# Optimization experiments

Hardware: AMD Instinct MI355X
Metric: run time of the kernel (lower is better)

## Reference

```python
import jax, jax.numpy as jnp
import numpy as np

B, T, C, H, L, E, K, V = 4, 1024, 1024, 16, 2, 8, 2, 32000
HD = C // H
CAP = B * T * K // E  # expert capacity with capacity_factor=1.0 -> 2048


def setup_inputs() -> dict:
    key = jax.random.key(0)
    ks = iter(jax.random.split(key, 16))
    def rn(shape, s=0.02):
        return jax.random.normal(next(ks), shape, jnp.float32) * s
    return {
        'input_ids': jax.random.randint(next(ks), (B, T), 0, V),
        'noise': jax.random.normal(next(ks), (L, B, T, E), jnp.float32),
        'tok_emb': rn((V, C)),
        'pos_emb': rn((T, C)),
        'ln1_w': jnp.ones((L, C)), 'ln1_b': jnp.zeros((L, C)),
        'qkv_w': rn((L, 3 * C, C)), 'out_w': rn((L, C, C)),
        'ln2_w': jnp.ones((L, C)), 'ln2_b': jnp.zeros((L, C)),
        'rt_w': rn((L, E, C)), 'rt_b': jnp.zeros((L, E)),
        'nz_w': rn((L, E, C)), 'nz_b': jnp.zeros((L, E)),
        'e_w1': rn((L, E, 4 * C, C)), 'e_b1': jnp.zeros((L, E, 4 * C)),
        'e_w2': rn((L, E, C, 4 * C)), 'e_b2': jnp.zeros((L, E, C)),
        'lnf_w': jnp.ones((C,)), 'lnf_b': jnp.zeros((C,)),
        'head_w': rn((1, C)), 'head_b': jnp.zeros((1,)),
    }


def _ln(x, w, b):
    m = jnp.mean(x, -1, keepdims=True)
    v = jnp.mean(jnp.square(x - m), -1, keepdims=True)
    return (x - m) * jax.lax.rsqrt(v + 1e-5) * w + b


def _attn(x, qkv_w, out_w):
    # non-causal flash-attention equivalent (softmax_scale = 1/sqrt(head_size))
    qkv = (x @ qkv_w.T).reshape(B, T, 3, H, HD)
    q, k, v = qkv[:, :, 0], qkv[:, :, 1], qkv[:, :, 2]
    s = jnp.einsum('bthd,bshd->bhts', q, k) / np.float32(np.sqrt(HD))
    p = jax.nn.softmax(s, axis=-1)
    o = jnp.einsum('bhts,bshd->bthd', p, v).reshape(B, T, C)
    return o @ out_w.T


def _moe(x, rt_w, rt_b, nz_w, nz_b, w1, b1, w2, b2, noise):
    logits = x @ rt_w.T + rt_b                      # [B,T,E]
    noise_logits = x @ nz_w.T + nz_b
    noisy = logits + noise * jax.nn.softplus(noise_logits)
    topv, topi = jax.lax.top_k(noisy, K)            # [B,T,K]
    gates = jax.nn.softmax(topv, axis=-1)           # softmax over sparse (-inf filled) logits == softmax over top-k
    oh = jax.nn.one_hot(topi, E, dtype=x.dtype)     # [B,T,K,E]
    router = jnp.einsum('btk,btke->bte', gates, oh)
    N = B * T
    flat_x = x.reshape(N, C)
    flat_r = router.reshape(N, E)
    flat_i = topi.reshape(N, K)
    updates = jnp.zeros_like(flat_x)
    for i in range(E):  # per-expert gather -> FFN -> scatter, capacity-limited in token order
        mask = jnp.any(flat_i == i, axis=-1)        # [N]
        pos = jnp.cumsum(mask) - 1
        keep = mask & (pos < CAP)
        sel = jnp.argsort(jnp.logical_not(keep))[:CAP]  # stable: kept tokens first, original order
        valid = keep[sel].astype(x.dtype)
        xi = flat_x[sel]                             # [CAP,C]
        h = jax.nn.relu(xi @ w1[i].T + b1[i])
        out = h @ w2[i].T + b2[i]
        gate = flat_r[sel, i] * valid
        updates = updates.at[sel].add(out * gate[:, None])
    return updates.reshape(B, T, C)


def reference(input_ids, noise, tok_emb, pos_emb, ln1_w, ln1_b, qkv_w, out_w,
              ln2_w, ln2_b, rt_w, rt_b, nz_w, nz_b, e_w1, e_b1, e_w2, e_b2,
              lnf_w, lnf_b, head_w, head_b):
    x = tok_emb[input_ids] + pos_emb[None, :T]
    for l in range(L):
        x = x + _attn(_ln(x, ln1_w[l], ln1_b[l]), qkv_w[l], out_w[l])
        x = x + _moe(_ln(x, ln2_w[l], ln2_b[l]), rt_w[l], rt_b[l], nz_w[l], nz_b[l],
                     e_w1[l], e_b1[l], e_w2[l], e_b2[l], noise[l])
    x = _ln(x, lnf_w, lnf_b)
    return jnp.mean(x, axis=1) @ head_w.T + head_b  # [B,1]
```

## Files before the change

kernel.cpp:

```cpp
#include <hip/hip_runtime.h>
#include <hip/hip_bf16.h>
#include <math.h>

namespace {

constexpr int B = 4, T = 1024, C = 1024, Hh = 16, L = 2, E = 8, HD = 64;
constexpr int NTOK = B * T;
constexpr int CAP = 1024;
constexpr int C3 = 3 * C, C4 = 4 * C;

typedef __attribute__((ext_vector_type(8))) short bf16x8;
typedef __attribute__((ext_vector_type(8))) short short8;
typedef __attribute__((ext_vector_type(4))) float f32x4;

static __device__ __forceinline__ short f2b(float f) {
  __hip_bfloat16 h = __float2bfloat16(f);
  return *reinterpret_cast<short*>(&h);
}
static __device__ __forceinline__ float b2f(unsigned short u) {
  union { unsigned int i; float f; } v; v.i = (unsigned int)u << 16; return v.f;
}

#define SWZ(row, kb) (((row) << 7) + ((kb) ^ (((row) & 7) << 4)))

static __device__ __forceinline__ void gload16(const void* g, void* l) {
  __builtin_amdgcn_global_load_lds((const __attribute__((address_space(1))) void*)g,
                                   (__attribute__((address_space(3))) void*)l, 16, 0, 0);
}

__global__ __launch_bounds__(256) void cvt4_kernel(
    const float* __restrict__ s0, const float* __restrict__ s1,
    const float* __restrict__ s2, const float* __restrict__ s3,
    unsigned short* __restrict__ d0, unsigned short* __restrict__ d1,
    unsigned short* __restrict__ d2, unsigned short* __restrict__ d3) {
  constexpr size_t N0 = (size_t)L * C3 * C, N1 = (size_t)L * C * C;
  constexpr size_t N2 = (size_t)L * E * C4 * C;
  size_t i = ((size_t)blockIdx.x * 256 + threadIdx.x) * 16;
  const float* s; unsigned short* d; size_t off;
  if (i < N0)                { s = s0; d = d0; off = i; }
  else if (i < N0 + N1)      { s = s1; d = d1; off = i - N0; }
  else if (i < N0 + N1 + N2) { s = s2; d = d2; off = i - N0 - N1; }
  else                       { s = s3; d = d3; off = i - N0 - N1 - N2; }
  f32x4 v0 = __builtin_nontemporal_load((const f32x4*)(s + off));
  f32x4 v1 = __builtin_nontemporal_load((const f32x4*)(s + off + 4));
  f32x4 v2 = __builtin_nontemporal_load((const f32x4*)(s + off + 8));
  f32x4 v3 = __builtin_nontemporal_load((const f32x4*)(s + off + 12));
  short8 r0, r1;
  r0[0] = f2b(v0[0]); r0[1] = f2b(v0[1]); r0[2] = f2b(v0[2]); r0[3] = f2b(v0[3]);
  r0[4] = f2b(v1[0]); r0[5] = f2b(v1[1]); r0[6] = f2b(v1[2]); r0[7] = f2b(v1[3]);
  r1[0] = f2b(v2[0]); r1[1] = f2b(v2[1]); r1[2] = f2b(v2[2]); r1[3] = f2b(v2[3]);
  r1[4] = f2b(v3[0]); r1[5] = f2b(v3[1]); r1[6] = f2b(v3[2]); r1[7] = f2b(v3[3]);
  __builtin_nontemporal_store(r0, (short8*)(d + off));
  __builtin_nontemporal_store(r1, (short8*)(d + off + 8));
}

__global__ __launch_bounds__(256) void embed_ln_kernel(const int* __restrict__ ids,
    const float* __restrict__ tok, const float* __restrict__ pos,
    float* __restrict__ x, unsigned short* __restrict__ outb,
    const float* __restrict__ w, const float* __restrict__ b) {
  __shared__ float red[8];
  int row = blockIdx.x, tid = threadIdx.x;
  int t = row & (T - 1);
  int id = ids[row];
  float4 a = ((const float4*)(tok + (size_t)id * C))[tid];
  float4 p = ((const float4*)(pos + (size_t)t * C))[tid];
  float4 v{a.x + p.x, a.y + p.y, a.z + p.z, a.w + p.w};
  ((float4*)(x + (size_t)row * C))[tid] = v;
  float s = v.x + v.y + v.z + v.w;
  #pragma unroll
  for (int off = 32; off > 0; off >>= 1) s += __shfl_down(s, off);
  if ((tid & 63) == 0) red[tid >> 6] = s;
  __syncthreads();
  float mean = (red[0] + red[1] + red[2] + red[3]) * (1.f / C);
  __syncthreads();
  float dx = v.x - mean, dy = v.y - mean, dz = v.z - mean, dw = v.w - mean;
  float sq = dx * dx + dy * dy + dz * dz + dw * dw;
  #pragma unroll
  for (int off = 32; off > 0; off >>= 1) sq += __shfl_down(sq, off);
  if ((tid & 63) == 0) red[tid >> 6] = sq;
  __syncthreads();
  float var = (red[0] + red[1] + red[2] + red[3]) * (1.f / C);
  float rs = rsqrtf(var + 1e-5f);
  float4 wc = ((const float4*)w)[tid];
  float4 bc = ((const float4*)b)[tid];
  short4 ob{f2b(dx * rs * wc.x + bc.x), f2b(dy * rs * wc.y + bc.y),
            f2b(dz * rs * wc.z + bc.z), f2b(dw * rs * wc.w + bc.w)};
  *(short4*)(outb + (size_t)row * C + tid * 4) = ob;
}

__global__ __launch_bounds__(256) void ln_kernel(const float* __restrict__ in,
    const unsigned short* __restrict__ eo, const int* __restrict__ slot0,
    const int* __restrict__ slot1, float* __restrict__ xupd,
    float* __restrict__ out, unsigned short* __restrict__ outb,
    const float* __restrict__ w, const float* __restrict__ b) {
  constexpr size_t SLICE = (size_t)E * CAP * C;
  __shared__ float red[8];
  int row = blockIdx.x, tid = threadIdx.x;
  float4 v = ((const float4*)(in + (size_t)row * C))[tid];
  if (eo) {
    int s0 = slot0[row], s1 = slot1[row];
    auto addslot = [&](int s) {
      if (s < 0) return;
      const unsigned short* p0 = eo + (size_t)s * C + tid * 4;
      short4 u = *(const short4*)p0;
      short4 u2 = *(const short4*)(p0 + SLICE);
      v.x += b2f((unsigned short)u.x) + b2f((unsigned short)u2.x);
      v.y += b2f((unsigned short)u.y) + b2f((unsigned short)u2.y);
      v.z += b2f((unsigned short)u.z) + b2f((unsigned short)u2.z);
      v.w += b2f((unsigned short)u.w) + b2f((unsigned short)u2.w);
    };
    addslot(s0);
    addslot(s1);
    if (xupd) ((float4*)(xupd + (size_t)row * C))[tid] = v;
  }
  float s = v.x + v.y + v.z + v.w;
  #pragma unroll
  for (int off = 32; off > 0; off >>= 1) s += __shfl_down(s, off);
  if ((tid & 63) == 0) red[tid >> 6] = s;
  __syncthreads();
  float mean = (red[0] + red[1] + red[2] + red[3]) * (1.f / C);
  __syncthreads();
  float dx = v.x - mean, dy = v.y - mean, dz = v.z - mean, dw = v.w - mean;
  float sq = dx * dx + dy * dy + dz * dz + dw * dw;
  #pragma unroll
  for (int off = 32; off > 0; off >>= 1) sq += __shfl_down(sq, off);
  if ((tid & 63) == 0) red[tid >> 6] = sq;
  __syncthreads();
  float var = (red[0] + red[1] + red[2] + red[3]) * (1.f / C);
  float rs = rsqrtf(var + 1e-5f);
  float4 wc = ((const float4*)w)[tid];
  float4 bc = ((const float4*)b)[tid];
  float4 o{dx * rs * wc.x + bc.x, dy * rs * wc.y + bc.y,
           dz * rs * wc.z + bc.z, dw * rs * wc.w + bc.w};
  if (out) ((float4*)(out + (size_t)row * C))[tid] = o;
  if (outb) {
    short4 ob{f2b(o.x), f2b(o.y), f2b(o.z), f2b(o.w)};
    *(short4*)(outb + (size_t)row * C + tid * 4) = ob;
  }
}

__global__ __launch_bounds__(256) void ln2_router_kernel(const float* __restrict__ in,
    unsigned short* __restrict__ outb,
    const float* __restrict__ w, const float* __restrict__ b,
    const float* __restrict__ rt_w, const float* __restrict__ rt_b,
    const float* __restrict__ nz_w, const float* __restrict__ nz_b,
    const float* __restrict__ noise,
    int* __restrict__ i0, int* __restrict__ i1, float* __restrict__ g0,
    float* __restrict__ g1, int* __restrict__ slot0, int* __restrict__ slot1)
{
  __shared__ float red[8];
  __shared__ float racc[4][16];
  int row = blockIdx.x, tid = threadIdx.x;
  float4 v = ((const float4*)(in + (size_t)row * C))[tid];
  float s = v.x + v.y + v.z + v.w;
  #pragma unroll
  for (int off = 32; off > 0; off >>= 1) s += __shfl_down(s, off);
  if ((tid & 63) == 0) red[tid >> 6] = s;
  __syncthreads();
  float mean = (red[0] + red[1] + red[2] + red[3]) * (1.f / C);
  __syncthreads();
  float dx = v.x - mean, dy = v.y - mean, dz = v.z - mean, dw = v.w - mean;
  float sq = dx * dx + dy * dy + dz * dz + dw * dw;
  #pragma unroll
  for (int off = 32; off > 0; off >>= 1) sq += __shfl_down(sq, off);
  if ((tid & 63) == 0) red[tid >> 6] = sq;
  __syncthreads();
  float var = (red[0] + red[1] + red[2] + red[3]) * (1.f / C);
  float rs = rsqrtf(var + 1e-5f);
  float4 wc = ((const float4*)w)[tid];
  float4 bc = ((const float4*)b)[tid];
  float4 o{dx * rs * wc.x + bc.x, dy * rs * wc.y + bc.y,
           dz * rs * wc.z + bc.z, dw * rs * wc.w + bc.w};
  short4 ob{f2b(o.x), f2b(o.y), f2b(o.z), f2b(o.w)};
  *(short4*)(outb + (size_t)row * C + tid * 4) = ob;

  float loc[16];
  #pragma unroll
  for (int e = 0; e < 8; e++) {
    float4 rw = *(const float4*)(rt_w + (size_t)e * C + tid * 4);
    float4 nw = *(const float4*)(nz_w + (size_t)e * C + tid * 4);
    loc[e]     = o.x * rw.x + o.y * rw.y + o.z * rw.z + o.w * rw.w;
    loc[8 + e] = o.x * nw.x + o.y * nw.y + o.z * nw.z + o.w * nw.w;
  }
  #pragma unroll
  for (int e = 0; e < 16; e++) {
    #pragma unroll
    for (int off = 32; off > 0; off >>= 1) loc[e] += __shfl_down(loc[e], off);
  }
  if ((tid & 63) == 0) {
    #pragma unroll
    for (int e = 0; e < 16; e++) racc[tid >> 6][e] = loc[e];
  }
  __syncthreads();
  if (tid == 0) {
    float nv[8];
    #pragma unroll
    for (int e = 0; e < 8; e++) {
      float lgt = racc[0][e] + racc[1][e] + racc[2][e] + racc[3][e] + rt_b[e];
      float nl = racc[0][8 + e] + racc[1][8 + e] + racc[2][8 + e] + racc[3][8 + e] + nz_b[e];
      float sp = fmaxf(nl, 0.f) + log1pf(expf(-fabsf(nl)));
      nv[e] = lgt + noise[(size_t)row * E + e] * sp;
    }
    float v0 = -INFINITY, v1 = -INFINITY; int b0 = -1, b1 = -1;
    #pragma unroll
    for (int e = 0; e < 8; e++) {
      float vv = nv[e];
      if (vv > v0)      { v1 = v0; b1 = b0; v0 = vv; b0 = e; }
      else if (vv > v1) { v1 = vv; b1 = e; }
    }
    float ex = expf(v1 - v0);
    float inv = 1.f / (1.f + ex);
    i0[row] = b0; i1[row] = b1;
    g0[row] = inv; g1[row] = ex * inv;
    slot0[row] = -1; slot1[row] = -1;
  }
}

template<bool GATHER, bool RELU, bool BIAS, bool XCDMAP, int OUTMODE, int SPLITK>
__global__ __launch_bounds__(512, 2) void gemm8p(
    const unsigned short* __restrict__ A, const unsigned short* __restrict__ W,
    const float* __restrict__ bias, unsigned short* __restrict__ Cout,
    const int* __restrict__ rowidx, const float* __restrict__ rowscale,
    const int* __restrict__ cnts, int M, int N, int Kd,
    size_t strideA, size_t strideW, size_t strideOut, int strideBias, int GY)
{
  __shared__ alignas(16) char smem[131072];
  int bx, by, e, ksl;
  if constexpr (XCDMAP) {
    int fid = blockIdx.x; e = fid & 7; int r1 = fid >> 3;
    ksl = r1 & (SPLITK - 1); int wi = r1 / SPLITK;
    by = wi % GY; bx = wi / GY;
  } else { bx = blockIdx.x; by = blockIdx.y; e = 0; ksl = 0; }
  int Mr = M;
  if (cnts) { int cc = cnts[e]; Mr = cc < M ? cc : M; }
  int row0 = by * 256, col0 = bx * 256;
  if (row0 >= Mr) return;

  const int kLen = Kd / SPLITK;
  const unsigned short* Ap = A + (size_t)e * strideA;
  const unsigned short* Wp = W + (size_t)e * strideW;
  const int* ridx = rowidx ? rowidx + (size_t)e * CAP : nullptr;

  int t = threadIdx.x;
  int l = t & 63, lm = l & 15, lg = l >> 4;
  int w = t >> 6, wm = w >> 2, wn = w & 3;

  const char* srcA[2];
  const char* srcB[2];
  #pragma unroll
  for (int j = 0; j < 2; j++) {
    int flat = t + j * 512;
    int row = flat >> 2;
    int c16 = (flat & 3) ^ ((row >> 1) & 3);
    int ga;
    if constexpr (GATHER) {
      int ar = row0 + row; if (ar >= Mr) ar = Mr - 1; ga = ridx[ar];
    } else ga = row0 + row;
    srcA[j] = (const char*)Ap + (size_t)ga * Kd * 2 + (size_t)ksl * kLen * 2 + c16 * 16;
    srcB[j] = (const char*)Wp + (size_t)(col0 + row) * Kd * 2 + (size_t)ksl * kLen * 2 + c16 * 16;
  }
  int dst0 = t * 16, dst1 = t * 16 + 8192;

  auto STAGE = [&](int buf, int op, int kh, int kt) {
    size_t goff = (size_t)kt * 128 + kh * 64;
    char* base = smem + buf * 65536 + op * 32768 + kh * 16384;
    if (op) {
      gload16(srcB[0] + goff, base + dst0);
      gload16(srcB[1] + goff, base + dst1);
    } else {
      gload16(srcA[0] + goff, base + dst0);
      gload16(srcA[1] + goff, base + dst1);
    }
  };

  int colswz = (lg ^ ((lm >> 1) & 3)) * 16;

  f32x4 acc[8][4];
  #pragma unroll
  for (int i = 0; i < 8; i++)
    #pragma unroll
    for (int j = 0; j < 4; j++) acc[i][j] = f32x4{0.f, 0.f, 0.f, 0.f};

  STAGE(0, 0, 0, 0); STAGE(0, 1, 0, 0); STAGE(0, 0, 1, 0); STAGE(0, 1, 1, 0);
  asm volatile("s_waitcnt vmcnt(0)" ::: "memory");
  __builtin_amdgcn_s_barrier();

  int NT = kLen >> 6;
  bf16x8 bfr[4];
  for (int k = 0; k < NT; k++) {
    int cur = k & 1, nxt = cur ^ 1;
    bool pf = (k + 1 < NT);
    #pragma unroll
    for (int ph = 0; ph < 4; ph++) {
      const int ks = ph >> 1, mh = ph & 1;
      bf16x8 afr[4];
      #pragma unroll
      for (int i = 0; i < 4; i++) {
        int row = wm * 128 + (mh * 4 + i) * 16 + lm;
        afr[i] = *(const bf16x8*)(smem + cur * 65536 + ks * 16384 + row * 64 + colswz);
      }
      if (mh == 0) {
        #pragma unroll
        for (int i = 0; i < 4; i++) {
          int row = wn * 64 + i * 16 + lm;
          bfr[i] = *(const bf16x8*)(smem + cur * 65536 + 32768 + ks * 16384 + row * 64 + colswz);
        }
      }
      if (pf) STAGE(nxt, mh, ks, k + 1);
      if (mh == 1) {
        if (pf) asm volatile("s_waitcnt vmcnt(4)" ::: "memory");
        else    asm volatile("s_waitcnt vmcnt(0)" ::: "memory");
      }
      __builtin_amdgcn_s_barrier();
      __builtin_amdgcn_s_setprio(1);
      #pragma unroll
      for (int i = 0; i < 4; i++)
        #pragma unroll
        for (int ni = 0; ni < 4; ni++)
          acc[mh * 4 + i][ni] =
              __builtin_amdgcn_mfma_f32_16x16x32_bf16(afr[i], bfr[ni], acc[mh * 4 + i][ni], 0, 0, 0);
      __builtin_amdgcn_s_setprio(0);
      __builtin_amdgcn_s_barrier();
    }
  }

  float cbias[4];
  #pragma unroll
  for (int ni = 0; ni < 4; ni++)
    cbias[ni] = (BIAS && ksl == 0) ? bias[(size_t)e * strideBias + col0 + wn * 64 + ni * 16 + lm] : 0.f;

  #pragma unroll
  for (int mi = 0; mi < 8; mi++) {
    #pragma unroll
    for (int rr = 0; rr < 4; rr++) {
      int m = row0 + wm * 128 + mi * 16 + lg * 4 + rr;
      if (m >= Mr) continue;
      if constexpr (OUTMODE == 0) {
        unsigned short* cp = Cout + (size_t)e * strideOut + (size_t)m * N + col0 + wn * 64 + lm;
        #pragma unroll
        for (int ni = 0; ni < 4; ni++) {
          float v = acc[mi][ni][rr] + cbias[ni];
          if constexpr (RELU) v = fmaxf(v, 0.f);
          cp[ni * 16] = (unsigned short)f2b(v);
        }
      } else {
        float sc = rowscale[(size_t)e * CAP + m];
        unsigned short* cp = Cout + (size_t)ksl * ((size_t)E * CAP * N)
                             + ((size_t)e * CAP + m) * N + col0 + wn * 64 + lm;
        #pragma unroll
        for (int ni = 0; ni < 4; ni++) {
          float v = acc[mi][ni][rr] + cbias[ni];
          cp[ni * 16] = (unsigned short)f2b(sc * v);
        }
      }
    }
  }
}

__global__ __launch_bounds__(256) void gemm_proj(
    const unsigned short* __restrict__ A, const unsigned short* __restrict__ W,
    float* __restrict__ Cout, int M, int N, int Kd)
{
  int bx = blockIdx.x, by = blockIdx.y;
  int row0 = by * 128, col0 = bx * 128;

  __shared__ alignas(16) char smem[32768];
  char* Ab = smem;
  char* Bb = smem + 16384;

  int t = threadIdx.x, w = t >> 6, l = t & 63;
  int lm = l & 15, lg = l >> 4;
  int wr = w >> 1, wc = w & 1;

  int lrow8 = l >> 3;
  int scol = ((l & 7) ^ lrow8) << 4;
  const char* srcA[4];
  const char* srcB[4];
  #pragma unroll
  for (int i = 0; i < 4; i++) {
    int seg = w * 4 + i;
    int rloc = seg * 8 + lrow8;
    srcA[i] = (const char*)A + (size_t)(row0 + rloc) * Kd * 2 + scol;
    srcB[i] = (const char*)W + (size_t)(col0 + rloc) * Kd * 2 + scol;
  }

  f32x4 acc[4][4];
  #pragma unroll
  for (int i = 0; i < 4; i++)
    #pragma unroll
    for (int j = 0; j < 4; j++) acc[i][j] = f32x4{0.f, 0.f, 0.f, 0.f};

  int NT = Kd >> 6;
  for (int kt = 0; kt < NT; kt++) {
    __syncthreads();
    #pragma unroll
    for (int i = 0; i < 4; i++) {
      int seg = w * 4 + i;
      gload16(srcA[i], Ab + seg * 1024);
      gload16(srcB[i], Bb + seg * 1024);
      srcA[i] += 128;
      srcB[i] += 128;
    }
    __syncthreads();
    #pragma unroll
    for (int ks = 0; ks < 2; ks++) {
      bf16x8 af[4], bfr[4];
      #pragma unroll
      for (int mi = 0; mi < 4; mi++)
        af[mi] = *(const bf16x8*)(Ab + SWZ(wr * 64 + mi * 16 + lm, ks * 64 + lg * 16));
      #pragma unroll
      for (int ni = 0; ni < 4; ni++)
        bfr[ni] = *(const bf16x8*)(Bb + SWZ(wc * 64 + ni * 16 + lm, ks * 64 + lg * 16));
      #pragma unroll
      for (int mi = 0; mi < 4; mi++)
        #pragma unroll
        for (int ni = 0; ni < 4; ni++)
          acc[mi][ni] = __builtin_amdgcn_mfma_f32_16x16x32_bf16(af[mi], bfr[ni], acc[mi][ni], 0, 0, 0);
    }
  }

  #pragma unroll
  for (int mi = 0; mi < 4; mi++) {
    #pragma unroll
    for (int rr = 0; rr < 4; rr++) {
      int m = row0 + wr * 64 + mi * 16 + lg * 4 + rr;
      float* cp = Cout + (size_t)m * N + col0 + wc * 64 + lm;
      #pragma unroll
      for (int ni = 0; ni < 4; ni++) cp[ni * 16] += acc[mi][ni][rr];
    }
  }
}

__global__ __launch_bounds__(256) void attn_mfma(const unsigned short* __restrict__ qkv,
                                                 unsigned short* __restrict__ ao) {
  __shared__ alignas(16) char smem[20480];
  char* Ks = smem;
  char* Vt = smem + 4096;
  char* Pb = smem + 12288;

  int t = threadIdx.x, w = t >> 6, lane = t & 63, lm = lane & 15, lg = lane >> 4;
  int qt = blockIdx.x, bh = blockIdx.y, b = bh >> 4, h = bh & 15;
  const unsigned short* base = qkv + (size_t)b * T * C3;

  bf16x8 qf[2];
  {
    int qrow = qt * 64 + w * 16 + lm;
    const unsigned short* qp = base + (size_t)qrow * C3 + h * HD + lg * 8;
    qf[0] = *(const bf16x8*)qp;
    qf[1] = *(const bf16x8*)(qp + 32);
  }

  f32x4 o[4];
  #pragma unroll
  for (int i = 0; i < 4; i++) o[i] = f32x4{0.f, 0.f, 0.f, 0.f};
  float mrun[4] = {-INFINITY, -INFINITY, -INFINITY, -INFINITY};
  float lpart[4] = {0.f, 0.f, 0.f, 0.f};

  int ksrow = t >> 3, kc = (t & 7) * 8;
  int vdl = t & 7;
  bf16x8 kreg;
  unsigned short vv[8];
  auto LOADKV = [&](int s0) {
    kreg = *(const bf16x8*)(base + (size_t)(s0 + ksrow) * C3 + C + h * HD + kc);
    const unsigned short* vp = base + (size_t)(s0 + ksrow) * C3 + 2 * C + h * HD + vdl;
    #pragma unroll
    for (int i = 0; i < 8; i++) vv[i] = vp[8 * i];
  };

  LOADKV(0);
  for (int s0 = 0; s0 < T; s0 += 32) {
    __syncthreads();
    *(bf16x8*)(Ks + SWZ(ksrow, kc * 2)) = kreg;
    #pragma unroll
    for (int i = 0; i < 8; i++) {
      int d = 8 * i + vdl;
      *(short*)(Vt + (d << 7) + ((ksrow * 2) ^ ((d & 7) << 4))) = (short)vv[i];
    }
    __syncthreads();
    if (s0 + 32 < T) LOADKV(s0 + 32);

    f32x4 sacc[2];
    sacc[0] = f32x4{0.f, 0.f, 0.f, 0.f};
    sacc[1] = f32x4{0.f, 0.f, 0.f, 0.f};
    #pragma unroll
    for (int ni = 0; ni < 2; ni++)
      #pragma unroll
      for (int ks = 0; ks < 2; ks++) {
        bf16x8 kfrag = *(const bf16x8*)(Ks + SWZ(ni * 16 + lm, ks * 64 + lg * 16));
        sacc[ni] = __builtin_amdgcn_mfma_f32_16x16x32_bf16(qf[ks], kfrag, sacc[ni], 0, 0, 0);
      }

    float sv0[4], sv1[4], pv[8];
    bool okd = true;
    #pragma unroll
    for (int r = 0; r < 4; r++) {
      sv0[r] = sacc[0][r] * 0.125f;
      sv1[r] = sacc[1][r] * 0.125f;
      okd = okd && (fmaxf(sv0[r], sv1[r]) <= mrun[r] + 8.f);
    }
    if (__all(okd ? 1 : 0)) {
      #pragma unroll
      for (int r = 0; r < 4; r++) {
        float p0 = __expf(sv0[r] - mrun[r]);
        float p1 = __expf(sv1[r] - mrun[r]);
        lpart[r] += p0 + p1;
        pv[r] = p0; pv[4 + r] = p1;
      }
    } else {
      float fr[4];
      #pragma unroll
      for (int r = 0; r < 4; r++) {
        float tmax = fmaxf(sv0[r], sv1[r]);
        #pragma unroll
        for (int mk = 1; mk < 16; mk <<= 1) tmax = fmaxf(tmax, __shfl_xor(tmax, mk));
        float mn = fmaxf(mrun[r], tmax);
        float f = __expf(mrun[r] - mn);
        float p0 = __expf(sv0[r] - mn), p1 = __expf(sv1[r] - mn);
        lpart[r] = lpart[r] * f + p0 + p1;
        mrun[r] = mn;
        fr[r] = f;
        pv[r] = p0; pv[4 + r] = p1;
      }
      #pragma unroll
      for (int ni = 0; ni < 4; ni++) {
        o[ni][0] *= fr[0]; o[ni][1] *= fr[1]; o[ni][2] *= fr[2]; o[ni][3] *= fr[3];
      }
    }

    char* P = Pb + w * 2048;
    #pragma unroll
    for (int ni = 0; ni < 2; ni++)
      #pragma unroll
      for (int r = 0; r < 4; r++) {
        int q = lg * 4 + r;
        int kbyte = (ni * 16 + lm) * 2;
        *(short*)(P + (q << 7) + (kbyte ^ ((q & 7) << 4))) = f2b(pv[ni * 4 + r]);
      }
    bf16x8 pfrag = *(const bf16x8*)(P + SWZ(lm, lg * 16));
    #pragma unroll
    for (int ni = 0; ni < 4; ni++) {
      bf16x8 vfrag = *(const bf16x8*)(Vt + SWZ(ni * 16 + lm, lg * 16));
      o[ni] = __builtin_amdgcn_mfma_f32_16x16x32_bf16(pfrag, vfrag, o[ni], 0, 0, 0);
    }
  }

  float inv[4];
  #pragma unroll
  for (int r = 0; r < 4; r++) {
    float lsum = lpart[r];
    #pragma unroll
    for (int mk = 1; mk < 16; mk <<= 1) lsum += __shfl_xor(lsum, mk);
    inv[r] = 1.f / lsum;
  }
  #pragma unroll
  for (int r = 0; r < 4; r++) {
    int qrow = qt * 64 + w * 16 + lg * 4 + r;
    unsigned short* dst = ao + (size_t)(b * T + qrow) * C + h * HD + lm;
    #pragma unroll
    for (int ni = 0; ni < 4; ni++) dst[ni * 16] = (unsigned short)f2b(o[ni][r] * inv[r]);
  }
}

__global__ __launch_bounds__(512) void capacity_kernel(
    const int* __restrict__ i0, const int* __restrict__ i1,
    const float* __restrict__ g0, const float* __restrict__ g1,
    int* __restrict__ sel, float* __restrict__ gsel, int* __restrict__ counts,
    int* __restrict__ slot0, int* __restrict__ slot1)
{
  int e = threadIdx.x >> 6, lane = threadIdx.x & 63;
  int cnt = 0;
  unsigned long long ltmask = (lane == 0) ? 0ull : (~0ull >> (64 - lane));
  int a = i0[lane], bb = i1[lane];
  for (int basei = 0; basei < NTOK; basei += 64) {
    int na = 0, nb = 0;
    if (basei + 64 < NTOK) { na = i0[basei + 64 + lane]; nb = i1[basei + 64 + lane]; }
    int tt = basei + lane;
    bool match = (a == e) || (bb == e);
    unsigned long long mk = __ballot(match);
    int pos = cnt + __popcll(mk & ltmask);
    if (match && pos < CAP) {
      sel[e * CAP + pos] = tt;
      gsel[e * CAP + pos] = (a == e) ? g0[tt] : g1[tt];
      if (a == e) slot0[tt] = e * CAP + pos;
      else        slot1[tt] = e * CAP + pos;
    }
    cnt += __popcll(mk);
    a = na; bb = nb;
  }
  if (lane == 0) counts[e] = cnt < CAP ? cnt : CAP;
}

__global__ __launch_bounds__(256) void head_part(const float* __restrict__ xin,
    const float* __restrict__ hw, float* __restrict__ partial)
{
  __shared__ float red[8];
  int blk = blockIdx.x;
  int b = blk >> 4, j = blk & 15;
  int tid = threadIdx.x;
  float4 wv = ((const float4*)hw)[tid];
  float s = 0.f;
  int t0 = j * 64;
  for (int t = t0; t < t0 + 64; t++) {
    float4 v = ((const float4*)(xin + (size_t)(b * T + t) * C))[tid];
    s += v.x * wv.x + v.y * wv.y + v.z * wv.z + v.w * wv.w;
  }
  #pragma unroll
  for (int off = 32; off > 0; off >>= 1) s += __shfl_down(s, off);
  if ((tid & 63) == 0) red[tid >> 6] = s;
  __syncthreads();
  if (tid == 0) partial[blk] = red[0] + red[1] + red[2] + red[3];
}

__global__ __launch_bounds__(64) void head_final(const float* __restrict__ partial,
    const float* __restrict__ hb, float* __restrict__ out)
{
  int tid = threadIdx.x;
  float v = partial[tid];
  #pragma unroll
  for (int off = 8; off > 0; off >>= 1) v += __shfl_down(v, off, 16);
  if ((tid & 15) == 0) out[tid >> 4] = v * (1.f / T) + hb[0];
}

}

extern "C" void kernel_launch(void* const* d_in, const int* in_sizes, int n_in,
                              void* d_out, int out_size, void* d_ws, size_t ws_size,
                              hipStream_t stream) {
  (void)in_sizes; (void)n_in; (void)out_size; (void)ws_size;
  const int*   ids     = (const int*)d_in[0];
  const float* noise   = (const float*)d_in[1];
  const float* tok_emb = (const float*)d_in[2];
  const float* pos_emb = (const float*)d_in[3];
  const float* ln1_w   = (const float*)d_in[4];
  const float* ln1_b   = (const float*)d_in[5];
  const float* qkv_w   = (const float*)d_in[6];
  const float* out_w   = (const float*)d_in[7];
  const float* ln2_w   = (const float*)d_in[8];
  const float* ln2_b   = (const float*)d_in[9];
  const float* rt_w    = (const float*)d_in[10];
  const float* rt_b    = (const float*)d_in[11];
  const float* nz_w    = (const float*)d_in[12];
  const float* nz_b    = (const float*)d_in[13];
  const float* e_w1    = (const float*)d_in[14];
  const float* e_b1    = (const float*)d_in[15];
  const float* e_w2    = (const float*)d_in[16];
  const float* e_b2    = (const float*)d_in[17];
  const float* lnf_w   = (const float*)d_in[18];
  const float* lnf_b   = (const float*)d_in[19];
  const float* head_w  = (const float*)d_in[20];
  const float* head_b  = (const float*)d_in[21];
  float* out = (float*)d_out;

  char* wsp = (char*)d_ws;
  size_t off = 0;
  auto alloc = [&](size_t n) { char* p = wsp + off; off += (n + 255) & ~(size_t)255; return p; };
  float* x    = (float*)alloc((size_t)NTOK * C * 4);
  float* t1   = (float*)alloc((size_t)NTOK * C * 4);
  unsigned short* t1b  = (unsigned short*)alloc((size_t)NTOK * C * 2);
  unsigned short* qkvb = (unsigned short*)alloc((size_t)NTOK * C3 * 2);
  unsigned short* aob  = (unsigned short*)alloc((size_t)NTOK * C * 2);
  unsigned short* hbuf = (unsigned short*)alloc((size_t)E * CAP * C4 * 2);
  unsigned short* eo   = (unsigned short*)alloc((size_t)2 * E * CAP * C * 2);
  unsigned short* qkvw_b = (unsigned short*)alloc((size_t)L * C3 * C * 2);
  unsigned short* outw_b = (unsigned short*)alloc((size_t)L * C * C * 2);
  unsigned short* ew1_b  = (unsigned short*)alloc((size_t)L * E * C4 * C * 2);
  unsigned short* ew2_b  = (unsigned short*)alloc((size_t)L * E * C * C4 * 2);
  int*   i0   = (int*)alloc(NTOK * 4);
  int*   i1   = (int*)alloc(NTOK * 4);
  float* g0   = (float*)alloc(NTOK * 4);
  float* g1   = (float*)alloc(NTOK * 4);
  int*   sel  = (int*)alloc(E * CAP * 4);
  float* gsel = (float*)alloc(E * CAP * 4);
  int*   counts = (int*)alloc(E * 4);
  int*   slot0  = (int*)alloc(NTOK * 4);
  int*   slot1  = (int*)alloc(NTOK * 4);
  float* hpart  = (float*)alloc(B * 16 * 4);

  {
    constexpr size_t TOT = (size_t)L * C3 * C + (size_t)L * C * C + 2 * (size_t)L * E * C4 * C;
    cvt4_kernel<<<(int)(TOT / 4096), 256, 0, stream>>>(qkv_w, out_w, e_w1, e_w2,
                                                       qkvw_b, outw_b, ew1_b, ew2_b);
  }

  for (int l = 0; l < L; l++) {
    if (l == 0)
      embed_ln_kernel<<<NTOK, 256, 0, stream>>>(ids, tok_emb, pos_emb, x, t1b,
                                                ln1_w, ln1_b);
    else
      ln_kernel<<<NTOK, 256, 0, stream>>>(x, eo, slot0, slot1, x,
                                          nullptr, t1b, ln1_w + l * C, ln1_b + l * C);
    gemm8p<false, false, false, false, 0, 1><<<dim3(C3 / 256, NTOK / 256), 512, 0, stream>>>(
        t1b, qkvw_b + (size_t)l * C3 * C, nullptr, qkvb,
        nullptr, nullptr, nullptr, NTOK, C3, C, 0, 0, 0, 0, 0);
    attn_mfma<<<dim3(T / 64, B * Hh), 256, 0, stream>>>(qkvb, aob);
    gemm_proj<<<dim3(C / 128, NTOK / 128), 256, 0, stream>>>(
        aob, outw_b + (size_t)l * C * C, x, NTOK, C, C);

    ln2_router_kernel<<<NTOK, 256, 0, stream>>>(x, t1b, ln2_w + l * C, ln2_b + l * C,
        rt_w + (size_t)l * E * C, rt_b + l * E, nz_w + (size_t)l * E * C, nz_b + l * E,
        noise + (size_t)l * NTOK * E, i0, i1, g0, g1, slot0, slot1);
    capacity_kernel<<<1, 512, 0, stream>>>(i0, i1, g0, g1, sel, gsel, counts, slot0, slot1);

    gemm8p<true, true, true, true, 0, 1><<<(C4 / 256) * (CAP / 256) * E, 512, 0, stream>>>(
        t1b, ew1_b + (size_t)l * E * C4 * C, e_b1 + (size_t)l * E * C4, hbuf,
        sel, nullptr, counts, CAP, C4, C,
        0, (size_t)C4 * C, (size_t)CAP * C4, C4, CAP / 256);
    gemm8p<false, false, true, true, 2, 2><<<(C / 256) * (CAP / 256) * 2 * E, 512, 0, stream>>>(
        hbuf, ew2_b + (size_t)l * E * C * C4, e_b2 + (size_t)l * E * C, eo,
        nullptr, gsel, counts, CAP, C, C4,
        (size_t)CAP * C4, (size_t)C * C4, 0, C, CAP / 256);
  }

  ln_kernel<<<NTOK, 256, 0, stream>>>(x, eo, slot0, slot1, nullptr,
                                      t1, nullptr, lnf_w, lnf_b);
  head_part<<<B * 16, 256, 0, stream>>>(t1, head_w, hpart);
  head_final<<<1, 64, 0, stream>>>(hpart, head_b, out);
}
```

Baseline: 890.1 us.

## Fuse fp32-to-bf16 expert weight conversion into MoE GEMM B-tile loads

Drops the separate pass that converted expert FFN weights to bf16. A new GEMM kernel loads fp32 weight tiles into registers, packs them to bf16 and writes them swizzled into LDS, double-buffered against MFMA work. This removes a large write and re-read of converted weights from the conversion kernel. In exchange, it uses 128-row M tiles, so the fp32 weights are re-fetched by more row tiles, and register pressure and conversion ALU work rise inside the GEMM.

```diff
diff --git a/kernel.cpp b/kernel.cpp
--- a/kernel.cpp
+++ b/kernel.cpp
@@ -20,6 +20,12 @@
 static __device__ __forceinline__ float b2f(unsigned short u) {
   union { unsigned int i; float f; } v; v.i = (unsigned int)u << 16; return v.f;
 }
+static __device__ __forceinline__ bf16x8 pack8(float4 a, float4 b) {
+  bf16x8 r;
+  r[0] = f2b(a.x); r[1] = f2b(a.y); r[2] = f2b(a.z); r[3] = f2b(a.w);
+  r[4] = f2b(b.x); r[5] = f2b(b.y); r[6] = f2b(b.z); r[7] = f2b(b.w);
+  return r;
+}
 
 #define SWZ(row, kb) (((row) << 7) + ((kb) ^ (((row) & 7) << 4)))
 
@@ -28,30 +34,25 @@
                                    (__attribute__((address_space(3))) void*)l, 16, 0, 0);
 }
 
-__global__ __launch_bounds__(256) void cvt4_kernel(
+__global__ __launch_bounds__(256) void cvt2_kernel(
     const float* __restrict__ s0, const float* __restrict__ s1,
-    const float* __restrict__ s2, const float* __restrict__ s3,
-    unsigned short* __restrict__ d0, unsigned short* __restrict__ d1,
-    unsigned short* __restrict__ d2, unsigned short* __restrict__ d3) {
-  constexpr size_t N0 = (size_t)L * C3 * C, N1 = (size_t)L * C * C;
-  constexpr size_t N2 = (size_t)L * E * C4 * C;
+    unsigned short* __restrict__ d0, unsigned short* __restrict__ d1) {
+  constexpr size_t N0 = (size_t)L * C3 * C;
   size_t i = ((size_t)blockIdx.x * 256 + threadIdx.x) * 16;
   const float* s; unsigned short* d; size_t off;
-  if (i < N0)                { s = s0; d = d0; off = i; }
-  else if (i < N0 + N1)      { s = s1; d = d1; off = i - N0; }
-  else if (i < N0 + N1 + N2) { s = s2; d = d2; off = i - N0 - N1; }
-  else                       { s = s3; d = d3; off = i - N0 - N1 - N2; }
-  f32x4 v0 = __builtin_nontemporal_load((const f32x4*)(s + off));
-  f32x4 v1 = __builtin_nontemporal_load((const f32x4*)(s + off + 4));
-  f32x4 v2 = __builtin_nontemporal_load((const f32x4*)(s + off + 8));
-  f32x4 v3 = __builtin_nontemporal_load((const f32x4*)(s + off + 12));
+  if (i < N0) { s = s0; d = d0; off = i; }
+  else        { s = s1; d = d1; off = i - N0; }
+  float4 v0 = *(const float4*)(s + off);
+  float4 v1 = *(const float4*)(s + off + 4);
+  float4 v2 = *(const float4*)(s + off + 8);
+  float4 v3 = *(const float4*)(s + off + 12);
   short8 r0, r1;
-  r0[0] = f2b(v0[0]); r0[1] = f2b(v0[1]); r0[2] = f2b(v0[2]); r0[3] = f2b(v0[3]);
-  r0[4] = f2b(v1[0]); r0[5] = f2b(v1[1]); r0[6] = f2b(v1[2]); r0[7] = f2b(v1[3]);
-  r1[0] = f2b(v2[0]); r1[1] = f2b(v2[1]); r1[2] = f2b(v2[2]); r1[3] = f2b(v2[3]);
-  r1[4] = f2b(v3[0]); r1[5] = f2b(v3[1]); r1[6] = f2b(v3[2]); r1[7] = f2b(v3[3]);
-  __builtin_nontemporal_store(r0, (short8*)(d + off));
-  __builtin_nontemporal_store(r1, (short8*)(d + off + 8));
+  r0[0] = f2b(v0.x); r0[1] = f2b(v0.y); r0[2] = f2b(v0.z); r0[3] = f2b(v0.w);
+  r0[4] = f2b(v1.x); r0[5] = f2b(v1.y); r0[6] = f2b(v1.z); r0[7] = f2b(v1.w);
+  r1[0] = f2b(v2.x); r1[1] = f2b(v2.y); r1[2] = f2b(v2.z); r1[3] = f2b(v2.w);
+  r1[4] = f2b(v3.x); r1[5] = f2b(v3.y); r1[6] = f2b(v3.z); r1[7] = f2b(v3.w);
+  *(short8*)(d + off) = r0;
+  *(short8*)(d + off + 8) = r1;
 }
 
 __global__ __launch_bounds__(256) void embed_ln_kernel(const int* __restrict__ ids,
@@ -334,6 +335,190 @@
     #pragma unroll
     for (int rr = 0; rr < 4; rr++) {
       int m = row0 + wm * 128 + mi * 16 + lg * 4 + rr;
+      if (m >= Mr) continue;
+      if constexpr (OUTMODE == 0) {
+        unsigned short* cp = Cout + (size_t)e * strideOut + (size_t)m * N + col0 + wn * 64 + lm;
+        #pragma unroll
+        for (int ni = 0; ni < 4; ni++) {
+          float v = acc[mi][ni][rr] + cbias[ni];
+          if constexpr (RELU) v = fmaxf(v, 0.f);
+          cp[ni * 16] = (unsigned short)f2b(v);
+        }
+      } else {
+        float sc = rowscale[(size_t)e * CAP + m];
+        unsigned short* cp = Cout + (size_t)ksl * ((size_t)E * CAP * N)
+                             + ((size_t)e * CAP + m) * N + col0 + wn * 64 + lm;
+        #pragma unroll
+        for (int ni = 0; ni < 4; ni++) {
+          float v = acc[mi][ni][rr] + cbias[ni];
+          cp[ni * 16] = (unsigned short)f2b(sc * v);
+        }
+      }
+    }
+  }
+}
+
+template<bool GATHER, bool RELU, bool BIAS, int OUTMODE, int SPLITK>
+__global__ __launch_bounds__(512, 2) void gemm_wf32(
+    const unsigned short* __restrict__ A, const float* __restrict__ W,
+    const float* __restrict__ bias, unsigned short* __restrict__ Cout,
+    const int* __restrict__ rowidx, const float* __restrict__ rowscale,
+    const int* __restrict__ cnts, int M, int N, int Kd,
+    size_t strideA, size_t strideW, size_t strideOut, int strideBias, int GY)
+{
+  __shared__ alignas(16) char smem[98304];
+  int fid = blockIdx.x;
+  int e = fid & 7; int r1 = fid >> 3;
+  int ksl = r1 & (SPLITK - 1); int wi = r1 / SPLITK;
+  int by = wi % GY, bx = wi / GY;
+  int Mr = M;
+  if (cnts) { int cc = cnts[e]; Mr = cc < M ? cc : M; }
+  int row0 = by * 128, col0 = bx * 256;
+  if (row0 >= Mr) return;
+
+  const int kLen = Kd / SPLITK;
+  const unsigned short* Ap = A + (size_t)e * strideA;
+  const float* Wp = W + (size_t)e * strideW;
+  const int* ridx = rowidx ? rowidx + (size_t)e * CAP : nullptr;
+
+  int t = threadIdx.x;
+  int l = t & 63, lm = l & 15, lg = l >> 4;
+  int w = t >> 6, wm = w >> 2, wn = w & 3;
+
+  int arow = t >> 2;
+  int ac16 = (t & 3) ^ ((arow >> 1) & 3);
+  int aga;
+  if constexpr (GATHER) {
+    int ar = row0 + arow; if (ar >= Mr) ar = Mr - 1; aga = ridx[ar];
+  } else aga = row0 + arow;
+  const char* srcA = (const char*)Ap + (size_t)aga * Kd * 2 + (size_t)ksl * kLen * 2 + ac16 * 16;
+  int adst = t * 16;
+  auto STAGEA = [&](int buf, int kt) {
+    size_t g = (size_t)kt * 128;
+    char* base = smem + buf * 49152;
+    gload16(srcA + g, base + adst);
+    gload16(srcA + g + 64, base + 8192 + adst);
+  };
+
+  int brow = t >> 1;
+  int bh2 = t & 1;
+  const float* bsrc = Wp + (size_t)(col0 + brow) * Kd + (size_t)ksl * kLen + bh2 * 32;
+  int bxor = ((brow >> 1) & 3) ^ (bh2 << 1);
+  float4 bregA[8], bregB[8];
+  auto LOADB_A = [&](int kt) {
+    const float* p = bsrc + (size_t)kt * 64;
+    #pragma unroll
+    for (int i = 0; i < 8; i++) bregA[i] = *(const float4*)(p + i * 4);
+  };
+  auto LOADB_B = [&](int kt) {
+    const float* p = bsrc + (size_t)kt * 64;
+    #pragma unroll
+    for (int i = 0; i < 8; i++) bregB[i] = *(const float4*)(p + i * 4);
+  };
+  auto WRITEB_A = [&](int buf) {
+    char* base = smem + buf * 49152 + 16384 + bh2 * 16384 + brow * 64;
+    #pragma unroll
+    for (int j = 0; j < 4; j++)
+      *(bf16x8*)(base + ((j ^ bxor) * 16)) = pack8(bregA[2 * j], bregA[2 * j + 1]);
+  };
+  auto WRITEB_B = [&](int buf) {
+    char* base = smem + buf * 49152 + 16384 + bh2 * 16384 + brow * 64;
+    #pragma unroll
+    for (int j = 0; j < 4; j++)
+      *(bf16x8*)(base + ((j ^ bxor) * 16)) = pack8(bregB[2 * j], bregB[2 * j + 1]);
+  };
+
+  int aswz = (lg ^ ((lm >> 1) & 3)) * 16;
+
+  f32x4 acc[4][4];
+  #pragma unroll
+  for (int i = 0; i < 4; i++)
+    #pragma unroll
+    for (int j = 0; j < 4; j++) acc[i][j] = f32x4{0.f, 0.f, 0.f, 0.f};
+
+  int NT = kLen >> 6;
+
+  LOADB_A(0);
+  STAGEA(0, 0);
+  LOADB_B(1);
+  WRITEB_A(0);
+  asm volatile("s_waitcnt vmcnt(8)" ::: "memory");
+  asm volatile("s_waitcnt lgkmcnt(0)" ::: "memory");
+  __builtin_amdgcn_s_barrier();
+
+  bf16x8 bfr[4];
+  auto TILE = [&](int cbase, auto stage_fn, auto write_fn) {
+    #pragma unroll
+    for (int ph = 0; ph < 4; ph++) {
+      const int ks = ph >> 1, mh = ph & 1;
+      bf16x8 afr[2];
+      #pragma unroll
+      for (int i = 0; i < 2; i++) {
+        int row = wm * 64 + (mh * 2 + i) * 16 + lm;
+        afr[i] = *(const bf16x8*)(smem + cbase + ks * 8192 + row * 64 + aswz);
+      }
+      if (mh == 0) {
+        int bswz = ((lg ^ ((lm >> 1) & 3)) ^ (ks << 1)) * 16;
+        #pragma unroll
+        for (int i = 0; i < 4; i++) {
+          int row = wn * 64 + i * 16 + lm;
+          bfr[i] = *(const bf16x8*)(smem + cbase + 16384 + ks * 16384 + row * 64 + bswz);
+        }
+      }
+      stage_fn(ph);
+      if (ph == 3) write_fn();
+      __builtin_amdgcn_s_barrier();
+      __builtin_amdgcn_s_setprio(1);
+      #pragma unroll
+      for (int i = 0; i < 2; i++)
+        #pragma unroll
+        for (int ni = 0; ni < 4; ni++)
+          acc[mh * 2 + i][ni] =
+              __builtin_amdgcn_mfma_f32_16x16x32_bf16(afr[i], bfr[ni], acc[mh * 2 + i][ni], 0, 0, 0);
+      __builtin_amdgcn_s_setprio(0);
+      __builtin_amdgcn_s_barrier();
+    }
+  };
+
+  for (int k = 0; k < NT; k += 2) {
+    bool pf2 = (k + 2 < NT);
+    bool pf3 = (k + 3 < NT);
+    TILE(0,
+      [&](int ph) {
+        if (ph == 0) STAGEA(1, k + 1);
+        if (ph == 1 && pf2) LOADB_A(k + 2);
+      },
+      [&]() {
+        WRITEB_B(1);
+        if (pf2) asm volatile("s_waitcnt vmcnt(8)" ::: "memory");
+        else     asm volatile("s_waitcnt vmcnt(0)" ::: "memory");
+        asm volatile("s_waitcnt lgkmcnt(0)" ::: "memory");
+      });
+    TILE(49152,
+      [&](int ph) {
+        if (ph == 0 && pf2) STAGEA(0, k + 2);
+        if (ph == 1 && pf3) LOADB_B(k + 3);
+      },
+      [&]() {
+        if (pf2) {
+          WRITEB_A(0);
+          if (pf3) asm volatile("s_waitcnt vmcnt(8)" ::: "memory");
+          else     asm volatile("s_waitcnt vmcnt(0)" ::: "memory");
+          asm volatile("s_waitcnt lgkmcnt(0)" ::: "memory");
+        }
+      });
+  }
+
+  float cbias[4];
+  #pragma unroll
+  for (int ni = 0; ni < 4; ni++)
+    cbias[ni] = (BIAS && ksl == 0) ? bias[(size_t)e * strideBias + col0 + wn * 64 + ni * 16 + lm] : 0.f;
+
+  #pragma unroll
+  for (int mi = 0; mi < 4; mi++) {
+    #pragma unroll
+    for (int rr = 0; rr < 4; rr++) {
+      int m = row0 + wm * 64 + mi * 16 + lg * 4 + rr;
       if (m >= Mr) continue;
       if constexpr (OUTMODE == 0) {
         unsigned short* cp = Cout + (size_t)e * strideOut + (size_t)m * N + col0 + wn * 64 + lm;
@@ -663,8 +848,6 @@
   unsigned short* eo   = (unsigned short*)alloc((size_t)2 * E * CAP * C * 2);
   unsigned short* qkvw_b = (unsigned short*)alloc((size_t)L * C3 * C * 2);
   unsigned short* outw_b = (unsigned short*)alloc((size_t)L * C * C * 2);
-  unsigned short* ew1_b  = (unsigned short*)alloc((size_t)L * E * C4 * C * 2);
-  unsigned short* ew2_b  = (unsigned short*)alloc((size_t)L * E * C * C4 * 2);
   int*   i0   = (int*)alloc(NTOK * 4);
   int*   i1   = (int*)alloc(NTOK * 4);
   float* g0   = (float*)alloc(NTOK * 4);
@@ -677,9 +860,8 @@
   float* hpart  = (float*)alloc(B * 16 * 4);
 
   {
-    constexpr size_t TOT = (size_t)L * C3 * C + (size_t)L * C * C + 2 * (size_t)L * E * C4 * C;
-    cvt4_kernel<<<(int)(TOT / 4096), 256, 0, stream>>>(qkv_w, out_w, e_w1, e_w2,
-                                                       qkvw_b, outw_b, ew1_b, ew2_b);
+    constexpr size_t TOT = (size_t)L * C3 * C + (size_t)L * C * C;
+    cvt2_kernel<<<(int)(TOT / 4096), 256, 0, stream>>>(qkv_w, out_w, qkvw_b, outw_b);
   }
 
   for (int l = 0; l < L; l++) {
@@ -701,14 +883,14 @@
         noise + (size_t)l * NTOK * E, i0, i1, g0, g1, slot0, slot1);
     capacity_kernel<<<1, 512, 0, stream>>>(i0, i1, g0, g1, sel, gsel, counts, slot0, slot1);
 
-    gemm8p<true, true, true, true, 0, 1><<<(C4 / 256) * (CAP / 256) * E, 512, 0, stream>>>(
-        t1b, ew1_b + (size_t)l * E * C4 * C, e_b1 + (size_t)l * E * C4, hbuf,
+    gemm_wf32<true, true, true, 0, 1><<<E * (CAP / 128) * (C4 / 256), 512, 0, stream>>>(
+        t1b, e_w1 + (size_t)l * E * C4 * C, e_b1 + (size_t)l * E * C4, hbuf,
         sel, nullptr, counts, CAP, C4, C,
-        0, (size_t)C4 * C, (size_t)CAP * C4, C4, CAP / 256);
-    gemm8p<false, false, true, true, 2, 2><<<(C / 256) * (CAP / 256) * 2 * E, 512, 0, stream>>>(
-        hbuf, ew2_b + (size_t)l * E * C * C4, e_b2 + (size_t)l * E * C, eo,
+        0, (size_t)C4 * C, (size_t)CAP * C4, C4, CAP / 128);
+    gemm_wf32<false, false, true, 2, 2><<<E * 2 * (CAP / 128) * (C / 256), 512, 0, stream>>>(
+        hbuf, e_w2 + (size_t)l * E * C * C4, e_b2 + (size_t)l * E * C, eo,
         nullptr, gsel, counts, CAP, C, C4,
-        (size_t)CAP * C4, (size_t)C * C4, 0, C, CAP / 256);
+        (size_t)CAP * C4, (size_t)C * C4, 0, C, CAP / 128);
   }
 
   ln_kernel<<<NTOK, 256, 0, stream>>>(x, eo, slot0, slot1, nullptr,
```

Result: slower. 1.199 ms (+34.7%).
